# Performance work log

Hardware: AMD Instinct MI355X
Metric: run time of the kernel (lower is better)

Reference implementation:

```python
import jax, jax.numpy as jnp
import numpy as np

C_IN, C_OUT, K, DG, PAD = 256, 256, 3, 2, 1
EPS = 1e-5


def setup_inputs() -> dict:
    key = jax.random.key(0)
    k = jax.random.split(key, 8)
    B, H, W = 4, 64, 64
    x = jax.random.normal(k[0], (B, C_IN, H, W), jnp.float32)
    # offset/mask conv (DCNv2 pack): 3 * dg * k * k output channels
    w_off = jax.random.normal(k[1], (3 * DG * K * K, C_IN, K, K), jnp.float32) * 0.01
    b_off = jnp.zeros((3 * DG * K * K,), jnp.float32)
    # main deformable conv weight
    w = jax.random.normal(k[2], (C_OUT, C_IN, K, K), jnp.float32) * (1.0 / np.sqrt(C_IN * K * K))
    b = jnp.zeros((C_OUT,), jnp.float32)
    # BatchNorm (eval mode: running stats)
    gamma = jnp.ones((C_OUT,), jnp.float32)
    beta = jnp.zeros((C_OUT,), jnp.float32)
    running_mean = jax.random.normal(k[3], (C_OUT,), jnp.float32) * 0.1
    running_var = jax.random.uniform(k[4], (C_OUT,), jnp.float32, 0.5, 1.5)
    return dict(x=x, w_off=w_off, b_off=b_off, w=w, b=b, gamma=gamma, beta=beta,
                running_mean=running_mean, running_var=running_var)


def _conv2d_same(x, w, b):
    y = jax.lax.conv_general_dilated(x, w, (1, 1), 'SAME',
                                     dimension_numbers=('NCHW', 'OIHW', 'NCHW'))
    return y + b[None, :, None, None]


def _deform_conv(x, w_off, b_off, w, b):
    B, C, H, W = x.shape
    K2 = K * K
    Cg = C // DG
    # offsets + modulation mask from internal conv (DCNv2 pack)
    om = _conv2d_same(x, w_off, b_off)            # [B, 3*DG*K2, H, W]
    o1, o2, m = jnp.split(om, 3, axis=1)
    mask = jax.nn.sigmoid(m).reshape(B, DG, 1, K2, H * W)
    off_y = o1.reshape(B, DG, K2, H, W)
    off_x = o2.reshape(B, DG, K2, H, W)
    # base sampling grid: output pixel + kernel tap - pad
    ki = jnp.arange(K)
    ky = (jnp.repeat(ki, K) - PAD).astype(jnp.float32)   # [K2]
    kx = (jnp.tile(ki, K) - PAD).astype(jnp.float32)     # [K2]
    py = off_y + ky[:, None, None] + jnp.arange(H, dtype=jnp.float32)[None, :, None]
    px = off_x + kx[:, None, None] + jnp.arange(W, dtype=jnp.float32)[None, None, :]
    y0 = jnp.floor(py)
    x0 = jnp.floor(px)
    ly = (py - y0).reshape(B, DG, 1, K2, H * W)
    lx = (px - x0).reshape(B, DG, 1, K2, H * W)
    y0i = y0.astype(jnp.int32)
    x0i = x0.astype(jnp.int32)
    xg = x.reshape(B, DG, Cg, H * W)

    def gather(yi, xi):
        # zero-padded bilinear corner gather, per deformable group
        valid = (yi >= 0) & (yi < H) & (xi >= 0) & (xi < W)
        lin = jnp.clip(yi, 0, H - 1) * W + jnp.clip(xi, 0, W - 1)
        v = jnp.take_along_axis(xg[:, :, :, None, :],
                                lin.reshape(B, DG, 1, K2, H * W), axis=-1)
        return v * valid.reshape(B, DG, 1, K2, H * W)

    val = (gather(y0i, x0i) * (1 - ly) * (1 - lx)
           + gather(y0i, x0i + 1) * (1 - ly) * lx
           + gather(y0i + 1, x0i) * ly * (1 - lx)
           + gather(y0i + 1, x0i + 1) * ly * lx)
    val = val * mask                               # [B, DG, Cg, K2, H*W]
    wr = w.reshape(C_OUT, DG, Cg, K2)
    out = jnp.einsum('bgckn,ogck->bon', val, wr).reshape(B, C_OUT, H, W)
    return out + b[None, :, None, None]


def reference(x, w_off, b_off, w, b, gamma, beta, running_mean, running_var):
    y = _deform_conv(x, w_off, b_off, w, b)
    inv = gamma / jnp.sqrt(running_var + EPS)
    y = (y - running_mean[None, :, None, None]) * inv[None, :, None, None] + beta[None, :, None, None]
    return jax.nn.relu(y)
```

## Files before the change

kernel.cpp:

```cpp
#include <hip/hip_runtime.h>
#include <math.h>

typedef __bf16 bf16x8 __attribute__((ext_vector_type(8)));
typedef float  f32x4  __attribute__((ext_vector_type(4)));
typedef int    i32x4  __attribute__((ext_vector_type(4)));

#define MFMA16(a, b, c) __builtin_amdgcn_mfma_f32_16x16x32_bf16((a), (b), (c), 0, 0, 0)

#define ATIDX(r, c) ((r) * 128 + (((c) ^ ((r) & 7)) * 8))

__global__ __launch_bounds__(256) void setup_kernel(
    const float* __restrict__ x, const float* __restrict__ w,
    const float* __restrict__ w_off, const float* __restrict__ bconv,
    const float* __restrict__ gamma, const float* __restrict__ beta,
    const float* __restrict__ mean, const float* __restrict__ var,
    __bf16* __restrict__ xT, __bf16* __restrict__ wFragD,
    __bf16* __restrict__ wFragO, float* __restrict__ sc,
    float* __restrict__ sh) {
  int t = threadIdx.x;
  if (blockIdx.x < 1024) {
    __shared__ float xs[64][65];
    int b = blockIdx.x >> 8, y = (blockIdx.x >> 2) & 63, cc = blockIdx.x & 3;
    for (int i = t; i < 4096; i += 256) {
      int cl = i >> 6, xc = i & 63;
      xs[cl][xc] = x[(((size_t)b * 256 + cc * 64 + cl) * 64 + y) * 64 + xc];
    }
    __syncthreads();
    for (int i = t; i < 4096; i += 256) {
      int xc = i >> 6, cl = i & 63;
      xT[(((size_t)b * 64 + y) * 64 + xc) * 256 + cc * 64 + cl] = (__bf16)xs[cl][xc];
    }
    return;
  }
  int i = (blockIdx.x - 1024) * 256 + t;
  if (i < 589824) {
    int j = i & 7, lane = (i >> 3) & 63, ocb = (i >> 9) & 15;
    int kc = (i >> 13) & 3, gk = i >> 15;
    int klocal = (lane >> 4) * 8 + j;
    int oc = ocb * 16 + (lane & 15);
    int c = kc * 32 + klocal;
    int g = gk / 9, ktap = gk % 9;
    wFragD[i] = (__bf16)w[((size_t)oc * 256 + g * 128 + c) * 9 + ktap];
  } else {
    int i2 = i - 589824;
    int j = i2 & 7, lane = (i2 >> 3) & 63, ocb = (i2 >> 9) & 3;
    int kc = (i2 >> 11) & 7, tap = i2 >> 14;
    int klocal = (lane >> 4) * 8 + j;
    int oc = ocb * 16 + (lane & 15);
    int ci = kc * 32 + klocal;
    wFragO[i2] = (oc < 54) ? (__bf16)w_off[((size_t)oc * 256 + ci) * 9 + tap]
                           : (__bf16)0.f;
  }
  if (i < 256) {
    float s = gamma[i] * rsqrtf(var[i] + 1e-5f);
    sc[i] = s;
    sh[i] = (bconv[i] - mean[i]) * s + beta[i];
  }
}

struct PhaseC {
  f32x4 swgtv[18 * 64];
  i32x4 slinv[18 * 64];
  __bf16 atile[2][2][64 * 128];
};
union FusedLDS {
  __bf16 rowbuf[3 * 66 * 256];
  PhaseC c;
};

__global__ __launch_bounds__(512) void fused_kernel(
    const __bf16* __restrict__ xT, const __bf16* __restrict__ wFragD,
    const __bf16* __restrict__ wFragO, const float* __restrict__ b_off,
    const float* __restrict__ sc, const float* __restrict__ sh,
    float* __restrict__ out) {
  __shared__ __attribute__((aligned(16))) FusedLDS U;
  __shared__ float omrow[54 * 64];
  int t = threadIdx.x;
  int b = blockIdx.x >> 6, y = blockIdx.x & 63;
  int lane = t & 63, wv = t >> 6;
  int l15 = lane & 15, quad = lane >> 4;
  const __bf16* xTb = xT + (size_t)b * 64 * 64 * 256;
  bf16x8 z8;
  #pragma unroll
  for (int e = 0; e < 8; ++e) z8[e] = (__bf16)0.f;

  for (int i = t; i < 3 * 66 * 32; i += 512) {
    int c = i & 31, px66 = (i >> 5) % 66, dy = i / 2112;
    int y2 = y + dy - 1, x2 = px66 - 1;
    bf16x8 v = z8;
    if (y2 >= 0 && y2 < 64 && x2 >= 0 && x2 < 64)
      v = *(const bf16x8*)(xTb + ((size_t)y2 * 64 + x2) * 256 + c * 8);
    *(bf16x8*)&U.rowbuf[dy * 16896 + px66 * 256 + ((c ^ (px66 & 7)) * 8)] = v;
  }
  __syncthreads();

  {
    int mh = wv & 1, ocq = wv >> 1;
    f32x4 acc0 = {0.f, 0.f, 0.f, 0.f};
    f32x4 acc1 = {0.f, 0.f, 0.f, 0.f};
    for (int tap = 0; tap < 9; ++tap) {
      int dy = tap / 3, dxs = tap % 3;
      const __bf16* bb = wFragO + ((size_t)(tap * 8) * 4 + ocq) * 512 + lane * 8;
      bf16x8 Bf[8];
      #pragma unroll
      for (int kc = 0; kc < 8; ++kc)
        Bf[kc] = *(const bf16x8*)(bb + (size_t)kc * 4 * 512);
      int p0 = mh * 32 + l15 + dxs, p1 = p0 + 16;
      const __bf16* rb = U.rowbuf + dy * 16896;
      #pragma unroll
      for (int kc = 0; kc < 8; ++kc) {
        int c = kc * 4 + quad;
        bf16x8 a0 = *(const bf16x8*)&rb[p0 * 256 + ((c ^ (p0 & 7)) * 8)];
        bf16x8 a1 = *(const bf16x8*)&rb[p1 * 256 + ((c ^ (p1 & 7)) * 8)];
        acc0 = MFMA16(a0, Bf[kc], acc0);
        acc1 = MFMA16(a1, Bf[kc], acc1);
      }
    }
    int oc = ocq * 16 + l15;
    if (oc < 54) {
      float bo = b_off[oc];
      #pragma unroll
      for (int fm = 0; fm < 2; ++fm) {
        f32x4 v = fm ? acc1 : acc0;
        f32x4 r = {v.x + bo, v.y + bo, v.z + bo, v.w + bo};
        int pxs = mh * 32 + fm * 16 + quad * 4;
        *(f32x4*)&omrow[oc * 64 + pxs] = r;
      }
    }
  }
  __syncthreads();

  for (int i = t; i < 18 * 64; i += 512) {
    int gk = i >> 6, p = i & 63;
    int k = gk % 9;
    float oy = omrow[gk * 64 + p];
    float ox = omrow[(18 + gk) * 64 + p];
    float mz = omrow[(36 + gk) * 64 + p];
    float mv = 1.f / (1.f + expf(-mz));
    float py  = (float)(y + (k / 3) - 1) + oy;
    float pxf = (float)(p + (k % 3) - 1) + ox;
    float y0f = floorf(py), x0f = floorf(pxf);
    int y0 = (int)y0f, x0 = (int)x0f;
    float ly = py - y0f, lx = pxf - x0f;
    int y1 = y0 + 1, x1 = x0 + 1;
    bool vy0 = (y0 >= 0) && (y0 < 64), vy1 = (y1 >= 0) && (y1 < 64);
    bool vx0 = (x0 >= 0) && (x0 < 64), vx1 = (x1 >= 0) && (x1 < 64);
    int cy0 = min(max(y0, 0), 63), cy1 = min(max(y1, 0), 63);
    int cx0 = min(max(x0, 0), 63), cx1 = min(max(x1, 0), 63);
    f32x4 sv;
    sv.x = (vy0 && vx0) ? (1.f - ly) * (1.f - lx) * mv : 0.f;
    sv.y = (vy0 && vx1) ? (1.f - ly) * lx * mv : 0.f;
    sv.z = (vy1 && vx0) ? ly * (1.f - lx) * mv : 0.f;
    sv.w = (vy1 && vx1) ? ly * lx * mv : 0.f;
    i32x4 lv;
    lv.x = (cy0 * 64 + cx0) * 256;
    lv.y = (cy0 * 64 + cx1) * 256;
    lv.z = (cy1 * 64 + cx0) * 256;
    lv.w = (cy1 * 64 + cx1) * 256;
    U.c.swgtv[i] = sv;
    U.c.slinv[i] = lv;
  }

  f32x4 acc[4][2];
  #pragma unroll
  for (int fm = 0; fm < 4; ++fm)
    #pragma unroll
    for (int fn = 0; fn < 2; ++fn)
      acc[fm][fn] = (f32x4){0.f, 0.f, 0.f, 0.f};

  __syncthreads();

  int ch0 = l15 * 8;
  #pragma unroll
  for (int t2 = 0; t2 < 2; ++t2) {
    const __bf16* xg = xTb + ch0;
    #pragma unroll
    for (int j = 0; j < 2; ++j) {
      int p = wv * 8 + j * 4 + quad;
      f32x4 sv = U.c.swgtv[t2 * 64 + p];
      i32x4 lv = U.c.slinv[t2 * 64 + p];
      bf16x8 c0 = *(const bf16x8*)(xg + lv.x);
      bf16x8 c1 = *(const bf16x8*)(xg + lv.y);
      bf16x8 c2 = *(const bf16x8*)(xg + lv.z);
      bf16x8 c3 = *(const bf16x8*)(xg + lv.w);
      bf16x8 o;
      #pragma unroll
      for (int e = 0; e < 8; ++e)
        o[e] = (__bf16)(sv.x * (float)c0[e] + sv.y * (float)c1[e]
                      + sv.z * (float)c2[e] + sv.w * (float)c3[e]);
      *(bf16x8*)&U.c.atile[0][t2][ATIDX(p, l15)] = o;
    }
  }

  for (int iv = 0; iv < 9; ++iv) {
    __syncthreads();
    bf16x8 Bf0[8], Bf1[8];
    {
      const __bf16* bb0 = wFragD + ((size_t)(2 * iv) * 4 * 16 + wv * 2) * 512 + lane * 8;
      const __bf16* bb1 = bb0 + (size_t)4 * 16 * 512;
      #pragma unroll
      for (int kc = 0; kc < 4; ++kc) {
        Bf0[kc * 2]     = *(const bf16x8*)(bb0 + (size_t)kc * 16 * 512);
        Bf0[kc * 2 + 1] = *(const bf16x8*)(bb0 + (size_t)kc * 16 * 512 + 512);
      }
      #pragma unroll
      for (int kc = 0; kc < 4; ++kc) {
        Bf1[kc * 2]     = *(const bf16x8*)(bb1 + (size_t)kc * 16 * 512);
        Bf1[kc * 2 + 1] = *(const bf16x8*)(bb1 + (size_t)kc * 16 * 512 + 512);
      }
    }
    bf16x8 cr[2][2][4];
    f32x4 sv[2][2];
    if (iv < 8) {
      #pragma unroll
      for (int t2 = 0; t2 < 2; ++t2) {
        int gn = 2 * iv + 2 + t2;
        const __bf16* xg = xTb + (gn / 9) * 128 + ch0;
        #pragma unroll
        for (int j = 0; j < 2; ++j) {
          int p = wv * 8 + j * 4 + quad;
          sv[t2][j] = U.c.swgtv[gn * 64 + p];
          i32x4 lv = U.c.slinv[gn * 64 + p];
          cr[t2][j][0] = *(const bf16x8*)(xg + lv.x);
          cr[t2][j][1] = *(const bf16x8*)(xg + lv.y);
          cr[t2][j][2] = *(const bf16x8*)(xg + lv.z);
          cr[t2][j][3] = *(const bf16x8*)(xg + lv.w);
        }
      }
    }
    __builtin_amdgcn_sched_barrier(0);
    {
      const __bf16* at0 = U.c.atile[iv & 1][0];
      #pragma unroll
      for (int kc = 0; kc < 4; ++kc) {
        #pragma unroll
        for (int fm = 0; fm < 4; ++fm) {
          bf16x8 a = *(const bf16x8*)&at0[ATIDX(fm * 16 + l15, kc * 4 + quad)];
          acc[fm][0] = MFMA16(a, Bf0[kc * 2],     acc[fm][0]);
          acc[fm][1] = MFMA16(a, Bf0[kc * 2 + 1], acc[fm][1]);
        }
      }
      const __bf16* at1 = U.c.atile[iv & 1][1];
      #pragma unroll
      for (int kc = 0; kc < 4; ++kc) {
        #pragma unroll
        for (int fm = 0; fm < 4; ++fm) {
          bf16x8 a = *(const bf16x8*)&at1[ATIDX(fm * 16 + l15, kc * 4 + quad)];
          acc[fm][0] = MFMA16(a, Bf1[kc * 2],     acc[fm][0]);
          acc[fm][1] = MFMA16(a, Bf1[kc * 2 + 1], acc[fm][1]);
        }
      }
    }
    __builtin_amdgcn_sched_barrier(0);
    if (iv < 8) {
      #pragma unroll
      for (int t2 = 0; t2 < 2; ++t2) {
        __bf16* dst = U.c.atile[(iv + 1) & 1][t2];
        #pragma unroll
        for (int j = 0; j < 2; ++j) {
          int p = wv * 8 + j * 4 + quad;
          bf16x8 o;
          #pragma unroll
          for (int e = 0; e < 8; ++e)
            o[e] = (__bf16)(sv[t2][j].x * (float)cr[t2][j][0][e]
                          + sv[t2][j].y * (float)cr[t2][j][1][e]
                          + sv[t2][j].z * (float)cr[t2][j][2][e]
                          + sv[t2][j].w * (float)cr[t2][j][3][e]);
          *(bf16x8*)&dst[ATIDX(p, l15)] = o;
        }
      }
    }
  }

  #pragma unroll
  for (int fm = 0; fm < 4; ++fm) {
    #pragma unroll
    for (int fn = 0; fn < 2; ++fn) {
      int oc = wv * 32 + fn * 16 + l15;
      float s = sc[oc], h = sh[oc];
      f32x4 v = acc[fm][fn];
      f32x4 r = {fmaxf(v.x * s + h, 0.f), fmaxf(v.y * s + h, 0.f),
                 fmaxf(v.z * s + h, 0.f), fmaxf(v.w * s + h, 0.f)};
      int pxs = fm * 16 + quad * 4;
      *(f32x4*)(out + (((size_t)b * 256 + oc) * 64 + y) * 64 + pxs) = r;
    }
  }
}

extern "C" void kernel_launch(void* const* d_in, const int* in_sizes, int n_in,
                              void* d_out, int out_size, void* d_ws, size_t ws_size,
                              hipStream_t stream) {
  const float* x     = (const float*)d_in[0];
  const float* w_off = (const float*)d_in[1];
  const float* b_off = (const float*)d_in[2];
  const float* w     = (const float*)d_in[3];
  const float* bconv = (const float*)d_in[4];
  const float* gamma = (const float*)d_in[5];
  const float* beta  = (const float*)d_in[6];
  const float* rmean = (const float*)d_in[7];
  const float* rvar  = (const float*)d_in[8];
  float* out = (float*)d_out;

  __bf16* xT     = (__bf16*)d_ws;
  __bf16* wFragD = (__bf16*)((char*)d_ws + 8388608);
  __bf16* wFragO = (__bf16*)((char*)d_ws + 9568256);
  float*  sc     = (float*)((char*)d_ws + 9863168);
  float*  sh     = (float*)((char*)d_ws + 9864192);

  setup_kernel<<<1024 + 2880, 256, 0, stream>>>(
      x, w, w_off, bconv, gamma, beta, rmean, rvar, xT, wFragD, wFragO, sc, sh);
  fused_kernel<<<4 * 64, 512, 0, stream>>>(xT, wFragD, wFragO, b_off, sc, sh, out);
}
```

Measured before the change: 131.0 us.

## Double fused block threads to 1024 and vectorize setup packing kernel

The fused kernel moves from 512 to 1024 threads per block. Each wave now owns 16 output channels instead of 32, and the offset-conv work is split across two K halves whose partial sums are reduced through a doubled omrow buffer, with the bias added at reduction time. The setup kernel is restructured so each thread reads float4 from x and writes bf16x8 vectors for the transpose and both weight-fragment packs, which cuts the grid from 3904 to 1385 blocks. The aim is more waves per CU to hide gather latency across only 256 blocks. The cost is extra barrier cost with twice the threads, more LDS, and repeated A-tile LDS reads per wave.

New measurement: 129.5 us. No clear change (-1.2%).

```diff
diff --git a/kernel.cpp b/kernel.cpp
--- a/kernel.cpp
+++ b/kernel.cpp
@@ -21,40 +21,60 @@
   if (blockIdx.x < 1024) {
     __shared__ float xs[64][65];
     int b = blockIdx.x >> 8, y = (blockIdx.x >> 2) & 63, cc = blockIdx.x & 3;
-    for (int i = t; i < 4096; i += 256) {
-      int cl = i >> 6, xc = i & 63;
-      xs[cl][xc] = x[(((size_t)b * 256 + cc * 64 + cl) * 64 + y) * 64 + xc];
+    const float* xb = x + (((size_t)b * 256 + cc * 64) * 64 + y) * 64;
+    #pragma unroll
+    for (int r = 0; r < 4; ++r) {
+      int cl = r * 16 + (t >> 4), xc = (t & 15) * 4;
+      f32x4 v = *(const f32x4*)(xb + (size_t)cl * 4096 + xc);
+      xs[cl][xc] = v.x; xs[cl][xc + 1] = v.y;
+      xs[cl][xc + 2] = v.z; xs[cl][xc + 3] = v.w;
     }
     __syncthreads();
-    for (int i = t; i < 4096; i += 256) {
-      int xc = i >> 6, cl = i & 63;
-      xT[(((size_t)b * 64 + y) * 64 + xc) * 256 + cc * 64 + cl] = (__bf16)xs[cl][xc];
+    __bf16* dst = xT + (((size_t)b * 64 + y) * 64) * 256 + cc * 64;
+    #pragma unroll
+    for (int it = 0; it < 2; ++it) {
+      int w2 = t + it * 256;
+      int xc = w2 >> 3, cl8 = (w2 & 7) * 8;
+      bf16x8 o;
+      #pragma unroll
+      for (int e = 0; e < 8; ++e) o[e] = (__bf16)xs[cl8 + e][xc];
+      *(bf16x8*)(dst + (size_t)xc * 256 + cl8) = o;
     }
     return;
   }
-  int i = (blockIdx.x - 1024) * 256 + t;
-  if (i < 589824) {
-    int j = i & 7, lane = (i >> 3) & 63, ocb = (i >> 9) & 15;
-    int kc = (i >> 13) & 3, gk = i >> 15;
-    int klocal = (lane >> 4) * 8 + j;
+  if (blockIdx.x < 1312) {
+    int u = (blockIdx.x - 1024) * 256 + t;
+    int lane = u & 63, ocb = (u >> 6) & 15, kc = (u >> 10) & 3, gk = u >> 12;
     int oc = ocb * 16 + (lane & 15);
-    int c = kc * 32 + klocal;
+    int cb = kc * 32 + (lane >> 4) * 8;
     int g = gk / 9, ktap = gk % 9;
-    wFragD[i] = (__bf16)w[((size_t)oc * 256 + g * 128 + c) * 9 + ktap];
-  } else {
-    int i2 = i - 589824;
-    int j = i2 & 7, lane = (i2 >> 3) & 63, ocb = (i2 >> 9) & 3;
-    int kc = (i2 >> 11) & 7, tap = i2 >> 14;
-    int klocal = (lane >> 4) * 8 + j;
-    int oc = ocb * 16 + (lane & 15);
-    int ci = kc * 32 + klocal;
-    wFragO[i2] = (oc < 54) ? (__bf16)w_off[((size_t)oc * 256 + ci) * 9 + tap]
-                           : (__bf16)0.f;
-  }
-  if (i < 256) {
-    float s = gamma[i] * rsqrtf(var[i] + 1e-5f);
-    sc[i] = s;
-    sh[i] = (bconv[i] - mean[i]) * s + beta[i];
+    const float* src = w + ((size_t)oc * 256 + g * 128 + cb) * 9 + ktap;
+    bf16x8 o;
+    #pragma unroll
+    for (int j = 0; j < 8; ++j) o[j] = (__bf16)src[(size_t)j * 9];
+    *(bf16x8*)(wFragD + (size_t)u * 8) = o;
+    return;
+  }
+  if (blockIdx.x < 1384) {
+    int u = (blockIdx.x - 1312) * 256 + t;
+    int lane = u & 63, ocq = (u >> 6) & 3, kc = (u >> 8) & 7, tap = u >> 11;
+    int oc = ocq * 16 + (lane & 15);
+    int cb = kc * 32 + (lane >> 4) * 8;
+    bf16x8 o;
+    #pragma unroll
+    for (int j = 0; j < 8; ++j) o[j] = (__bf16)0.f;
+    if (oc < 54) {
+      const float* src = w_off + ((size_t)oc * 256 + cb) * 9 + tap;
+      #pragma unroll
+      for (int j = 0; j < 8; ++j) o[j] = (__bf16)src[(size_t)j * 9];
+    }
+    *(bf16x8*)(wFragO + (size_t)u * 8) = o;
+    return;
+  }
+  if (t < 256) {
+    float s = gamma[t] * rsqrtf(var[t] + 1e-5f);
+    sc[t] = s;
+    sh[t] = (bconv[t] - mean[t]) * s + beta[t];
   }
 }
 
@@ -68,13 +88,13 @@
   PhaseC c;
 };
 
-__global__ __launch_bounds__(512) void fused_kernel(
+__global__ __launch_bounds__(1024) void fused_kernel(
     const __bf16* __restrict__ xT, const __bf16* __restrict__ wFragD,
     const __bf16* __restrict__ wFragO, const float* __restrict__ b_off,
     const float* __restrict__ sc, const float* __restrict__ sh,
     float* __restrict__ out) {
   __shared__ __attribute__((aligned(16))) FusedLDS U;
-  __shared__ float omrow[54 * 64];
+  __shared__ float omrow[2][54 * 64];
   int t = threadIdx.x;
   int b = blockIdx.x >> 6, y = blockIdx.x & 63;
   int lane = t & 63, wv = t >> 6;
@@ -84,7 +104,7 @@
   #pragma unroll
   for (int e = 0; e < 8; ++e) z8[e] = (__bf16)0.f;
 
-  for (int i = t; i < 3 * 66 * 32; i += 512) {
+  for (int i = t; i < 3 * 66 * 32; i += 1024) {
     int c = i & 31, px66 = (i >> 5) % 66, dy = i / 2112;
     int y2 = y + dy - 1, x2 = px66 - 1;
     bf16x8 v = z8;
@@ -95,47 +115,48 @@
   __syncthreads();
 
   {
-    int mh = wv & 1, ocq = wv >> 1;
+    int kh = wv & 1, ocq = (wv >> 1) & 3, mh = wv >> 3;
     f32x4 acc0 = {0.f, 0.f, 0.f, 0.f};
     f32x4 acc1 = {0.f, 0.f, 0.f, 0.f};
     for (int tap = 0; tap < 9; ++tap) {
       int dy = tap / 3, dxs = tap % 3;
-      const __bf16* bb = wFragO + ((size_t)(tap * 8) * 4 + ocq) * 512 + lane * 8;
-      bf16x8 Bf[8];
-      #pragma unroll
-      for (int kc = 0; kc < 8; ++kc)
-        Bf[kc] = *(const bf16x8*)(bb + (size_t)kc * 4 * 512);
+      const __bf16* bb =
+          wFragO + ((size_t)(tap * 8 + kh * 4) * 4 + ocq) * 512 + lane * 8;
+      bf16x8 Bf[4];
+      #pragma unroll
+      for (int kcl = 0; kcl < 4; ++kcl)
+        Bf[kcl] = *(const bf16x8*)(bb + (size_t)kcl * 4 * 512);
       int p0 = mh * 32 + l15 + dxs, p1 = p0 + 16;
       const __bf16* rb = U.rowbuf + dy * 16896;
       #pragma unroll
-      for (int kc = 0; kc < 8; ++kc) {
-        int c = kc * 4 + quad;
+      for (int kcl = 0; kcl < 4; ++kcl) {
+        int c = (kh * 4 + kcl) * 4 + quad;
         bf16x8 a0 = *(const bf16x8*)&rb[p0 * 256 + ((c ^ (p0 & 7)) * 8)];
         bf16x8 a1 = *(const bf16x8*)&rb[p1 * 256 + ((c ^ (p1 & 7)) * 8)];
-        acc0 = MFMA16(a0, Bf[kc], acc0);
-        acc1 = MFMA16(a1, Bf[kc], acc1);
+        acc0 = MFMA16(a0, Bf[kcl], acc0);
+        acc1 = MFMA16(a1, Bf[kcl], acc1);
       }
     }
     int oc = ocq * 16 + l15;
     if (oc < 54) {
-      float bo = b_off[oc];
       #pragma unroll
       for (int fm = 0; fm < 2; ++fm) {
         f32x4 v = fm ? acc1 : acc0;
-        f32x4 r = {v.x + bo, v.y + bo, v.z + bo, v.w + bo};
         int pxs = mh * 32 + fm * 16 + quad * 4;
-        *(f32x4*)&omrow[oc * 64 + pxs] = r;
+        *(f32x4*)&omrow[kh][oc * 64 + pxs] = v;
       }
     }
   }
   __syncthreads();
 
-  for (int i = t; i < 18 * 64; i += 512) {
+  for (int i = t; i < 18 * 64; i += 1024) {
     int gk = i >> 6, p = i & 63;
     int k = gk % 9;
-    float oy = omrow[gk * 64 + p];
-    float ox = omrow[(18 + gk) * 64 + p];
-    float mz = omrow[(36 + gk) * 64 + p];
+    float oy = omrow[0][gk * 64 + p] + omrow[1][gk * 64 + p] + b_off[gk];
+    float ox = omrow[0][(18 + gk) * 64 + p] + omrow[1][(18 + gk) * 64 + p]
+             + b_off[18 + gk];
+    float mz = omrow[0][(36 + gk) * 64 + p] + omrow[1][(36 + gk) * 64 + p]
+             + b_off[36 + gk];
     float mv = 1.f / (1.f + expf(-mz));
     float py  = (float)(y + (k / 3) - 1) + oy;
     float pxf = (float)(p + (k % 3) - 1) + ox;
@@ -161,71 +182,58 @@
     U.c.slinv[i] = lv;
   }
 
-  f32x4 acc[4][2];
+  f32x4 acc[4];
   #pragma unroll
-  for (int fm = 0; fm < 4; ++fm)
-    #pragma unroll
-    for (int fn = 0; fn < 2; ++fn)
-      acc[fm][fn] = (f32x4){0.f, 0.f, 0.f, 0.f};
+  for (int fm = 0; fm < 4; ++fm) acc[fm] = (f32x4){0.f, 0.f, 0.f, 0.f};
 
   __syncthreads();
 
   int ch0 = l15 * 8;
+  int p = wv * 4 + quad;
   #pragma unroll
   for (int t2 = 0; t2 < 2; ++t2) {
     const __bf16* xg = xTb + ch0;
-    #pragma unroll
-    for (int j = 0; j < 2; ++j) {
-      int p = wv * 8 + j * 4 + quad;
-      f32x4 sv = U.c.swgtv[t2 * 64 + p];
-      i32x4 lv = U.c.slinv[t2 * 64 + p];
-      bf16x8 c0 = *(const bf16x8*)(xg + lv.x);
-      bf16x8 c1 = *(const bf16x8*)(xg + lv.y);
-      bf16x8 c2 = *(const bf16x8*)(xg + lv.z);
-      bf16x8 c3 = *(const bf16x8*)(xg + lv.w);
-      bf16x8 o;
-      #pragma unroll
-      for (int e = 0; e < 8; ++e)
-        o[e] = (__bf16)(sv.x * (float)c0[e] + sv.y * (float)c1[e]
-                      + sv.z * (float)c2[e] + sv.w * (float)c3[e]);
-      *(bf16x8*)&U.c.atile[0][t2][ATIDX(p, l15)] = o;
-    }
+    f32x4 sv = U.c.swgtv[t2 * 64 + p];
+    i32x4 lv = U.c.slinv[t2 * 64 + p];
+    bf16x8 c0 = *(const bf16x8*)(xg + lv.x);
+    bf16x8 c1 = *(const bf16x8*)(xg + lv.y);
+    bf16x8 c2 = *(const bf16x8*)(xg + lv.z);
+    bf16x8 c3 = *(const bf16x8*)(xg + lv.w);
+    bf16x8 o;
+    #pragma unroll
+    for (int e = 0; e < 8; ++e)
+      o[e] = (__bf16)(sv.x * (float)c0[e] + sv.y * (float)c1[e]
+                    + sv.z * (float)c2[e] + sv.w * (float)c3[e]);
+    *(bf16x8*)&U.c.atile[0][t2][ATIDX(p, l15)] = o;
   }
 
   for (int iv = 0; iv < 9; ++iv) {
     __syncthreads();
-    bf16x8 Bf0[8], Bf1[8];
+    bf16x8 Bf0[4], Bf1[4];
     {
-      const __bf16* bb0 = wFragD + ((size_t)(2 * iv) * 4 * 16 + wv * 2) * 512 + lane * 8;
+      const __bf16* bb0 =
+          wFragD + ((size_t)(2 * iv) * 4 * 16 + wv) * 512 + lane * 8;
       const __bf16* bb1 = bb0 + (size_t)4 * 16 * 512;
       #pragma unroll
-      for (int kc = 0; kc < 4; ++kc) {
-        Bf0[kc * 2]     = *(const bf16x8*)(bb0 + (size_t)kc * 16 * 512);
-        Bf0[kc * 2 + 1] = *(const bf16x8*)(bb0 + (size_t)kc * 16 * 512 + 512);
-      }
-      #pragma unroll
-      for (int kc = 0; kc < 4; ++kc) {
-        Bf1[kc * 2]     = *(const bf16x8*)(bb1 + (size_t)kc * 16 * 512);
-        Bf1[kc * 2 + 1] = *(const bf16x8*)(bb1 + (size_t)kc * 16 * 512 + 512);
-      }
-    }
-    bf16x8 cr[2][2][4];
-    f32x4 sv[2][2];
+      for (int kc = 0; kc < 4; ++kc)
+        Bf0[kc] = *(const bf16x8*)(bb0 + (size_t)kc * 16 * 512);
+      #pragma unroll
+      for (int kc = 0; kc < 4; ++kc)
+        Bf1[kc] = *(const bf16x8*)(bb1 + (size_t)kc * 16 * 512);
+    }
+    bf16x8 cr[2][4];
+    f32x4 sv[2];
     if (iv < 8) {
       #pragma unroll
       for (int t2 = 0; t2 < 2; ++t2) {
         int gn = 2 * iv + 2 + t2;
         const __bf16* xg = xTb + (gn / 9) * 128 + ch0;
-        #pragma unroll
-        for (int j = 0; j < 2; ++j) {
-          int p = wv * 8 + j * 4 + quad;
-          sv[t2][j] = U.c.swgtv[gn * 64 + p];
-          i32x4 lv = U.c.slinv[gn * 64 + p];
-          cr[t2][j][0] = *(const bf16x8*)(xg + lv.x);
-          cr[t2][j][1] = *(const bf16x8*)(xg + lv.y);
-          cr[t2][j][2] = *(const bf16x8*)(xg + lv.z);
-          cr[t2][j][3] = *(const bf16x8*)(xg + lv.w);
-        }
+        sv[t2] = U.c.swgtv[gn * 64 + p];
+        i32x4 lv = U.c.slinv[gn * 64 + p];
+        cr[t2][0] = *(const bf16x8*)(xg + lv.x);
+        cr[t2][1] = *(const bf16x8*)(xg + lv.y);
+        cr[t2][2] = *(const bf16x8*)(xg + lv.z);
+        cr[t2][3] = *(const bf16x8*)(xg + lv.w);
       }
     }
     __builtin_amdgcn_sched_barrier(0);
@@ -236,8 +244,7 @@
         #pragma unroll
         for (int fm = 0; fm < 4; ++fm) {
           bf16x8 a = *(const bf16x8*)&at0[ATIDX(fm * 16 + l15, kc * 4 + quad)];
-          acc[fm][0] = MFMA16(a, Bf0[kc * 2],     acc[fm][0]);
-          acc[fm][1] = MFMA16(a, Bf0[kc * 2 + 1], acc[fm][1]);
+          acc[fm] = MFMA16(a, Bf0[kc], acc[fm]);
         }
       }
       const __bf16* at1 = U.c.atile[iv & 1][1];
@@ -246,8 +253,7 @@
         #pragma unroll
         for (int fm = 0; fm < 4; ++fm) {
           bf16x8 a = *(const bf16x8*)&at1[ATIDX(fm * 16 + l15, kc * 4 + quad)];
-          acc[fm][0] = MFMA16(a, Bf1[kc * 2],     acc[fm][0]);
-          acc[fm][1] = MFMA16(a, Bf1[kc * 2 + 1], acc[fm][1]);
+          acc[fm] = MFMA16(a, Bf1[kc], acc[fm]);
         }
       }
     }
@@ -256,29 +262,24 @@
       #pragma unroll
       for (int t2 = 0; t2 < 2; ++t2) {
         __bf16* dst = U.c.atile[(iv + 1) & 1][t2];
+        bf16x8 o;
         #pragma unroll
-        for (int j = 0; j < 2; ++j) {
-          int p = wv * 8 + j * 4 + quad;
-          bf16x8 o;
-          #pragma unroll
-          for (int e = 0; e < 8; ++e)
-            o[e] = (__bf16)(sv[t2][j].x * (float)cr[t2][j][0][e]
-                          + sv[t2][j].y * (float)cr[t2][j][1][e]
-                          + sv[t2][j].z * (float)cr[t2][j][2][e]
-                          + sv[t2][j].w * (float)cr[t2][j][3][e]);
-          *(bf16x8*)&dst[ATIDX(p, l15)] = o;
-        }
-      }
-    }
-  }
-
-  #pragma unroll
-  for (int fm = 0; fm < 4; ++fm) {
-    #pragma unroll
-    for (int fn = 0; fn < 2; ++fn) {
-      int oc = wv * 32 + fn * 16 + l15;
-      float s = sc[oc], h = sh[oc];
-      f32x4 v = acc[fm][fn];
+        for (int e = 0; e < 8; ++e)
+          o[e] = (__bf16)(sv[t2].x * (float)cr[t2][0][e]
+                        + sv[t2].y * (float)cr[t2][1][e]
+                        + sv[t2].z * (float)cr[t2][2][e]
+                        + sv[t2].w * (float)cr[t2][3][e]);
+        *(bf16x8*)&dst[ATIDX(p, l15)] = o;
+      }
+    }
+  }
+
+  {
+    int oc = wv * 16 + l15;
+    float s = sc[oc], h = sh[oc];
+    #pragma unroll
+    for (int fm = 0; fm < 4; ++fm) {
+      f32x4 v = acc[fm];
       f32x4 r = {fmaxf(v.x * s + h, 0.f), fmaxf(v.y * s + h, 0.f),
                  fmaxf(v.z * s + h, 0.f), fmaxf(v.w * s + h, 0.f)};
       int pxs = fm * 16 + quad * 4;
@@ -307,7 +308,7 @@
   float*  sc     = (float*)((char*)d_ws + 9863168);
   float*  sh     = (float*)((char*)d_ws + 9864192);
 
-  setup_kernel<<<1024 + 2880, 256, 0, stream>>>(
+  setup_kernel<<<1385, 256, 0, stream>>>(
       x, w, w_off, bconv, gamma, beta, rmean, rvar, xT, wFragD, wFragO, sc, sh);
-  fused_kernel<<<4 * 64, 512, 0, stream>>>(xT, wFragD, wFragO, b_off, sc, sh, out);
+  fused_kernel<<<4 * 64, 1024, 0, stream>>>(xT, wFragD, wFragO, b_off, sc, sh, out);
 }
```
